# Kernel optimization log

Hardware: AMD Instinct MI355X
Metric: run time of the kernel (lower is better)

Reference implementation:

```python
import jax, jax.numpy as jnp
import numpy as np

PS = 7  # patch (window) size
NH = 8  # num heads for local attention
EPS = 1e-5


def _rel_index(ps):
    # standard Swin-style relative position index over a ps x ps window
    coords = np.stack(np.meshgrid(np.arange(ps), np.arange(ps), indexing='ij'))  # (2,ps,ps)
    flat = coords.reshape(2, -1)                                # (2, ps*ps)
    rel = (flat[:, :, None] - flat[:, None, :]).transpose(1, 2, 0)  # (N,N,2)
    rel[..., 0] += ps - 1
    rel[..., 1] += ps - 1
    rel[..., 0] *= 2 * ps - 1
    return rel.sum(-1)  # (N,N) values in [0,(2ps-1)^2)

REL_IDX = jnp.asarray(_rel_index(PS))  # (49,49)


def _mha(x, qkv_w, qkv_b, proj_w, proj_b, num_heads, bias):
    # x: (Bn, N, C); weights stored (in,out)
    Bn, N, C = x.shape
    d = C // num_heads
    qkv = (x @ qkv_w + qkv_b).reshape(Bn, N, 3, num_heads, d).transpose(2, 0, 3, 1, 4)
    q, k, v = qkv[0], qkv[1], qkv[2]
    attn = jnp.einsum('bhnd,bhmd->bhnm', q, k) * (d ** -0.5)
    if bias is not None:
        attn = attn + bias
    attn = jax.nn.softmax(attn, axis=-1)
    out = jnp.einsum('bhnm,bhmd->bhnd', attn, v).transpose(0, 2, 1, 3).reshape(Bn, N, C)
    return out @ proj_w + proj_b


def setup_inputs() -> dict:
    key = jax.random.key(0)
    ks = jax.random.split(key, 8)
    B, C, H, W = 4, 256, 112, 112
    s = 0.02
    return {
        'x': jax.random.normal(ks[0], (B, C, H, W), jnp.float32),
        'norm_gamma': jnp.ones((C,), jnp.float32),
        'norm_beta': jnp.zeros((C,), jnp.float32),
        'qkv_l_w': jax.random.normal(ks[1], (C, 3 * C), jnp.float32) * s,
        'qkv_l_b': jnp.zeros((3 * C,), jnp.float32),
        'proj_l_w': jax.random.normal(ks[2], (C, C), jnp.float32) * s,
        'proj_l_b': jnp.zeros((C,), jnp.float32),
        'rpb_table': jax.random.normal(ks[3], ((2 * PS - 1) ** 2, NH), jnp.float32) * s,
        'qkv_c_w': jax.random.normal(ks[4], (PS * PS, 3 * PS * PS), jnp.float32) * s,
        'qkv_c_b': jnp.zeros((3 * PS * PS,), jnp.float32),
        'proj_c_w': jax.random.normal(ks[5], (PS * PS, PS * PS), jnp.float32) * s,
        'proj_c_b': jnp.zeros((PS * PS,), jnp.float32),
        'proj_w': jax.random.normal(ks[6], (2 * C, C), jnp.float32) * s,
    }


def reference(x, norm_gamma, norm_beta, qkv_l_w, qkv_l_b, proj_l_w, proj_l_b,
              rpb_table, qkv_c_w, qkv_c_b, proj_c_w, proj_c_b, proj_w):
    B, C, H, W = x.shape
    ps, N = PS, PS * PS
    nP = (H // ps) * (W // ps)
    shortcut = x

    # b c h w -> b h w c, then LayerNorm over C
    xt = x.transpose(0, 2, 3, 1)
    mu = xt.mean(-1, keepdims=True)
    var = xt.var(-1, keepdims=True)
    xn = (xt - mu) * jax.lax.rsqrt(var + EPS) * norm_gamma + norm_beta

    # window partition -> (B*nP, N, C)
    patches = xn.reshape(B, H // ps, ps, W // ps, ps, C)
    patches = patches.transpose(0, 1, 3, 2, 4, 5).reshape(-1, N, C)

    # local windowed attention with relative position bias
    bias = rpb_table[REL_IDX].transpose(2, 0, 1)[None]  # (1,NH,N,N)
    attn_local = _mha(patches, qkv_l_w, qkv_l_b, proj_l_w, proj_l_b, NH, bias)

    # cross-channel attention: (B*C, nP, N), dim=N, single head, no RPE
    pc = patches.reshape(B, nP, N, C).transpose(0, 3, 1, 2).reshape(B * C, nP, N)
    attn_cross = _mha(pc, qkv_c_w, qkv_c_b, proj_c_w, proj_c_b, 1, None)
    attn_cross = attn_cross.reshape(B, C, nP, N).transpose(0, 2, 3, 1).reshape(-1, N, C)

    def reverse(w):  # (B*nP, N, C) -> (B, H*W, C)
        w = w.reshape(B, H // ps, W // ps, ps, ps, C)
        return w.transpose(0, 1, 3, 2, 4, 5).reshape(B, H * W, C)

    out = jnp.concatenate([reverse(attn_local), reverse(attn_cross)], axis=-1) @ proj_w
    out = out.reshape(B, H, W, C).transpose(0, 3, 1, 2)
    return (out, shortcut)
```

## Files before the change

### kernel.cpp

```cpp
#include <hip/hip_runtime.h>
#include <hip/hip_bf16.h>


#define PS 7
#define NWIN_N 49
#define CH 256
#define HH 112
#define WW 112
#define BB 4
#define NHEAD 8
#define HD 32

static constexpr size_t ELEMS = (size_t)BB * CH * HH * WW;
static constexpr size_t SZ    = ELEMS * 2;

typedef __attribute__((ext_vector_type(8))) short short8;
typedef __attribute__((ext_vector_type(4))) float f32x4;

static __device__ __forceinline__ unsigned short bf16_bits(float v) {
    __hip_bfloat16 h = __float2bfloat16(v);
    return *reinterpret_cast<unsigned short*>(&h);
}

static __device__ __forceinline__ void gload_lds16(const void* g, void* l) {
    __builtin_amdgcn_global_load_lds(
        (const __attribute__((address_space(1))) unsigned int*)g,
        (__attribute__((address_space(3))) unsigned int*)l, 16, 0, 0);
}

__global__ __launch_bounds__(256) void ln_partition_kernel(
    const float* __restrict__ x, const float* __restrict__ gamma,
    const float* __restrict__ beta, __hip_bfloat16* __restrict__ patches)
{
    int blk = blockIdx.x;
    int seg = blk % 7;
    int bh = blk / 7;
    int h = bh % HH, b = bh / HH;
    int w0 = seg * 16;
    int tid = threadIdx.x;

    __shared__ float X[256][17];
    __shared__ float mus[16], rstds[16];

    #pragma unroll
    for (int l = 0; l < 16; ++l) {
        int idx = l * 256 + tid;
        int c = idx >> 4, wl = idx & 15;
        X[c][wl] = x[((size_t)(b * CH + c) * HH + h) * WW + w0 + wl];
    }
    __syncthreads();

    if (tid < 16) {
        float s = 0.f, ss = 0.f;
        for (int c = 0; c < 256; ++c) { float v = X[c][tid]; s += v; ss += v * v; }
        float mu = s * (1.f / 256.f);
        float var = ss * (1.f / 256.f) - mu * mu;
        mus[tid] = mu;
        rstds[tid] = rsqrtf(var + 1e-5f);
    }
    __syncthreads();

    int c = tid;
    float g = gamma[c], be = beta[c];
    int hp = h / PS, r = h - hp * PS;
    #pragma unroll
    for (int wl = 0; wl < 16; ++wl) {
        int w = w0 + wl;
        int wp = w / PS, cc = w - wp * PS;
        int win = (b * 16 + hp) * 16 + wp;
        int i = r * PS + cc;
        float v = (X[c][wl] - mus[wl]) * rstds[wl] * g + be;
        patches[((size_t)win * NWIN_N + i) * CH + c] = __float2bfloat16(v);
    }
}

__global__ __launch_bounds__(256) void copy_f32_kernel(
    const float* __restrict__ x, float* __restrict__ out)
{
    size_t i = ((size_t)blockIdx.x * 256 + threadIdx.x) * 4;
    *(float4*)(out + i) = *(const float4*)(x + i);
}

__global__ __launch_bounds__(256) void prep_wt_kernel(
    const float* __restrict__ W, unsigned short* __restrict__ Wt,
    int Kreal, int N, int Kpad, int Npad)
{
    int idx = blockIdx.x * 256 + threadIdx.x;
    if (idx >= Npad * Kpad) return;
    int n = idx / Kpad, k = idx - n * Kpad;
    float v = (n < N && k < Kreal) ? W[(size_t)k * N + n] : 0.f;
    Wt[idx] = bf16_bits(v);
}

__global__ __launch_bounds__(256) void prep_wt_qkvc_kernel(
    const float* __restrict__ W, unsigned short* __restrict__ Wt)
{
    int idx = blockIdx.x * 256 + threadIdx.x;
    if (idx >= 192 * 64) return;
    int n = idx >> 6, k = idx & 63;
    int s = -1;
    if (n < 49) s = n;
    else if (n >= 56 && n < 105) s = n - 7;
    else if (n >= 112 && n < 161) s = n - 14;
    float v = (s >= 0 && k < 49) ? W[(size_t)k * 147 + s] : 0.f;
    Wt[idx] = bf16_bits(v);
}

__global__ __launch_bounds__(192) void prep_bias_c_kernel(
    const float* __restrict__ b, float* __restrict__ bc)
{
    int n = threadIdx.x;
    int s = -1;
    if (n < 49) s = n;
    else if (n >= 56 && n < 105) s = n - 7;
    else if (n >= 112 && n < 161) s = n - 14;
    bc[n] = (s >= 0) ? b[s] : 0.f;
}

__global__ __launch_bounds__(256) void bias_prep_kernel(
    const float* __restrict__ rpb, float* __restrict__ biasb)
{
    int idx = blockIdx.x * 256 + threadIdx.x;
    int head = idx >> 12;
    int rem = idx & 4095;
    int i = rem >> 6, j = rem & 63;
    float v;
    if (j >= NWIN_N) v = -1e9f;
    else if (i >= NWIN_N) v = 0.f;
    else {
        int ri = i / 7, ci = i - ri * 7;
        int rj = j / 7, cj = j - rj * 7;
        v = rpb[((ri - rj + 6) * 13 + (ci - cj + 6)) * NHEAD + head];
    }
    biasb[idx] = v;
}

__global__ __launch_bounds__(256) void gemm_mfma_kernel(
    const __hip_bfloat16* __restrict__ A1p, const __hip_bfloat16* __restrict__ A2p,
    int K1, const unsigned short* __restrict__ Wt, const float* __restrict__ bias,
    __hip_bfloat16* __restrict__ Cb, float* __restrict__ Cf,
    int M, int N, int K, int pitchN)
{
    __shared__ __align__(16) unsigned short Alds[128 * 64];
    __shared__ __align__(16) unsigned short Wlds[64 * 64];
    const unsigned short* A1 = (const unsigned short*)A1p;
    const unsigned short* A2 = (const unsigned short*)A2p;

    const int nb = gridDim.x;
    const int ntiles = nb * gridDim.y;
    const int bid = blockIdx.y * nb + blockIdx.x;
    const int chunk = ntiles >> 3;
    const int tile = (bid & 7) * chunk + (bid >> 3);
    const int m0 = (tile / nb) * 128, n0 = (tile % nb) * 64;

    const int tid = threadIdx.x, lane = tid & 63, wave = tid >> 6;
    const int wm = wave >> 1, wn = wave & 1;
    const int lr = lane & 15, lk = lane >> 4;

    f32x4 acc[4][2];
    #pragma unroll
    for (int i = 0; i < 4; ++i)
        #pragma unroll
        for (int j = 0; j < 2; ++j) acc[i][j] = (f32x4){0.f, 0.f, 0.f, 0.f};

    for (int k0 = 0; k0 < K; k0 += 64) {
        #pragma unroll
        for (int i = 0; i < 4; ++i) {
            int s_lin = i * 256 + tid;
            int row = s_lin >> 3, sl = s_lin & 7;
            int c8 = ((sl ^ (row & 7)) << 3);
            int k = k0 + c8;
            const unsigned short* src = (k < K1)
                ? A1 + (size_t)(m0 + row) * K1 + k
                : A2 + (size_t)(m0 + row) * (K - K1) + (k - K1);
            gload_lds16(src, Alds + (size_t)(i * 256 + wave * 64) * 8);
        }
        #pragma unroll
        for (int i = 0; i < 2; ++i) {
            int s_lin = i * 256 + tid;
            int row = s_lin >> 3, sl = s_lin & 7;
            int c8 = ((sl ^ (row & 7)) << 3);
            gload_lds16(Wt + (size_t)(n0 + row) * K + k0 + c8,
                        Wlds + (size_t)(i * 256 + wave * 64) * 8);
        }
        __syncthreads();
        #pragma unroll
        for (int kk = 0; kk < 64; kk += 32) {
            short8 a[4], w[2];
            #pragma unroll
            for (int mi = 0; mi < 4; ++mi) {
                int r = wm * 64 + mi * 16 + lr;
                int sl = (kk >> 3) + lk;
                a[mi] = *(const short8*)&Alds[(r << 6) + (((sl) ^ (r & 7)) << 3)];
            }
            #pragma unroll
            for (int nj = 0; nj < 2; ++nj) {
                int r = wn * 32 + nj * 16 + lr;
                int sl = (kk >> 3) + lk;
                w[nj] = *(const short8*)&Wlds[(r << 6) + (((sl) ^ (r & 7)) << 3)];
            }
            #pragma unroll
            for (int mi = 0; mi < 4; ++mi)
                #pragma unroll
                for (int nj = 0; nj < 2; ++nj)
                    acc[mi][nj] = __builtin_amdgcn_mfma_f32_16x16x32_bf16(
                        a[mi], w[nj], acc[mi][nj], 0, 0, 0);
        }
        __syncthreads();
    }

    if (Cb) {
        if ((pitchN & 7) == 0) {
            #pragma unroll
            for (int nj = 0; nj < 2; ++nj) {
                int n = n0 + wn * 32 + nj * 16 + lr;
                float bv = (bias && n < N) ? bias[n] : 0.f;
                int col = wn * 32 + nj * 16 + lr;
                #pragma unroll
                for (int mi = 0; mi < 4; ++mi)
                    #pragma unroll
                    for (int r = 0; r < 4; ++r) {
                        int row = wm * 64 + mi * 16 + lk * 4 + r;
                        int idx = (row << 6) + (((col >> 3) ^ (row & 7)) << 3) + (col & 7);
                        Alds[idx] = bf16_bits(acc[mi][nj][r] + bv);
                    }
            }
            __syncthreads();
            #pragma unroll
            for (int i = 0; i < 4; ++i) {
                int s = tid + 256 * i;
                int row = s >> 3, sl = s & 7;
                if (n0 + sl * 8 + 8 <= pitchN)
                    *(short8*)((unsigned short*)Cb + (size_t)(m0 + row) * pitchN + n0 + sl * 8) =
                        *(const short8*)&Alds[(row << 6) + (((sl) ^ (row & 7)) << 3)];
            }
        } else {
            #pragma unroll
            for (int nj = 0; nj < 2; ++nj) {
                int n = n0 + wn * 32 + nj * 16 + lr;
                if (n >= N) continue;
                float bv = bias ? bias[n] : 0.f;
                #pragma unroll
                for (int mi = 0; mi < 4; ++mi) {
                    #pragma unroll
                    for (int r = 0; r < 4; ++r) {
                        int m = m0 + wm * 64 + mi * 16 + lk * 4 + r;
                        ((unsigned short*)Cb)[(size_t)m * pitchN + n] =
                            bf16_bits(acc[mi][nj][r] + bv);
                    }
                }
            }
        }
    } else {
        #pragma unroll
        for (int mi = 0; mi < 4; ++mi) {
            #pragma unroll
            for (int r = 0; r < 4; ++r) {
                int m = m0 + wm * 64 + mi * 16 + lk * 4 + r;
                int b = m / 12544, rem = m - b * 12544;
                int p = rem / 49, t = rem - p * 49;
                int h = (p >> 4) * 7 + t / 7, w = (p & 15) * 7 + (t % 7);
                size_t ob = ((size_t)(b * 256) * HH + h) * WW + w;
                #pragma unroll
                for (int nj = 0; nj < 2; ++nj) {
                    int ch = n0 + wn * 32 + nj * 16 + lr;
                    Cf[ob + (size_t)ch * (HH * WW)] = acc[mi][nj][r];
                }
            }
        }
    }
}

__global__ __launch_bounds__(64) void local_attn_mfma_kernel(
    const __hip_bfloat16* __restrict__ qkv,
    const float* __restrict__ biasb,
    __hip_bfloat16* __restrict__ outp)
{
    __shared__ __align__(16) unsigned short VT_lds[32][72];
    __shared__ __align__(16) unsigned short P_lds[16][72];

    const int win  = blockIdx.x >> 3;
    const int head = blockIdx.x & 7;
    const int lane = threadIdx.x;
    const int lr = lane & 15, lk = lane >> 4;
    const unsigned short* q16 = (const unsigned short*)qkv;
    const size_t rowbase = (size_t)win * NWIN_N;
    const float scale = 0.17677669529663687f;

    for (int t = 0; t < 32; ++t) {
        int idx = lane + 64 * t;
        int j = idx >> 5, d = idx & 31;
        unsigned short v = 0;
        if (j < NWIN_N) v = q16[(rowbase + j) * 768 + 512 + head * HD + d];
        VT_lds[d][j] = v;
    }

    short8 kf[4], qf[4];
    #pragma unroll
    for (int jt = 0; jt < 4; ++jt) {
        int j = jt * 16 + lr;
        short8 f = *(const short8*)(q16 + (rowbase + j) * 768 + 256 + head * HD + lk * 8);
        if (j >= NWIN_N) {
            #pragma unroll
            for (int e = 0; e < 8; ++e) f[e] = 0;
        }
        kf[jt] = f;
    }
    #pragma unroll
    for (int it = 0; it < 4; ++it) {
        int i = it * 16 + lr;
        qf[it] = *(const short8*)(q16 + (rowbase + i) * 768 + head * HD + lk * 8);
    }
    __syncthreads();

    #pragma unroll
    for (int it = 0; it < 4; ++it) {
        const int i = it * 16 + lr;
        f32x4 sacc[4];
        #pragma unroll
        for (int jt = 0; jt < 4; ++jt) {
            f32x4 z = (f32x4){0.f, 0.f, 0.f, 0.f};
            sacc[jt] = __builtin_amdgcn_mfma_f32_16x16x32_bf16(kf[jt], qf[it], z, 0, 0, 0);
        }
        const float* brow = biasb + head * 4096 + i * 64;
        float sv[4][4];
        float mt = -1e30f;
        #pragma unroll
        for (int jt = 0; jt < 4; ++jt) {
            float4 bv = *(const float4*)&brow[jt * 16 + lk * 4];
            sv[jt][0] = sacc[jt][0] * scale + bv.x;
            sv[jt][1] = sacc[jt][1] * scale + bv.y;
            sv[jt][2] = sacc[jt][2] * scale + bv.z;
            sv[jt][3] = sacc[jt][3] * scale + bv.w;
            #pragma unroll
            for (int r = 0; r < 4; ++r) mt = fmaxf(mt, sv[jt][r]);
        }
        mt = fmaxf(mt, __shfl_xor(mt, 16, 64));
        mt = fmaxf(mt, __shfl_xor(mt, 32, 64));
        float psum = 0.f;
        #pragma unroll
        for (int jt = 0; jt < 4; ++jt) {
            float p0 = __expf(sv[jt][0] - mt);
            float p1 = __expf(sv[jt][1] - mt);
            float p2 = __expf(sv[jt][2] - mt);
            float p3 = __expf(sv[jt][3] - mt);
            psum += (p0 + p1) + (p2 + p3);
            uint2 wv;
            wv.x = (unsigned)bf16_bits(p0) | ((unsigned)bf16_bits(p1) << 16);
            wv.y = (unsigned)bf16_bits(p2) | ((unsigned)bf16_bits(p3) << 16);
            *(uint2*)&P_lds[lr][jt * 16 + lk * 4] = wv;
        }
        psum += __shfl_xor(psum, 16, 64);
        psum += __shfl_xor(psum, 32, 64);
        __syncthreads();

        f32x4 oacc[2];
        oacc[0] = (f32x4){0.f, 0.f, 0.f, 0.f};
        oacc[1] = (f32x4){0.f, 0.f, 0.f, 0.f};
        #pragma unroll
        for (int kst = 0; kst < 2; ++kst) {
            short8 bfv = *(const short8*)&P_lds[lr][kst * 32 + lk * 8];
            #pragma unroll
            for (int dt = 0; dt < 2; ++dt) {
                short8 af = *(const short8*)&VT_lds[dt * 16 + lr][kst * 32 + lk * 8];
                oacc[dt] = __builtin_amdgcn_mfma_f32_16x16x32_bf16(af, bfv, oacc[dt], 0, 0, 0);
            }
        }
        if (i < NWIN_N) {
            float inv = 1.f / psum;
            unsigned short* orow = (unsigned short*)outp + (rowbase + i) * CH + head * HD;
            #pragma unroll
            for (int dt = 0; dt < 2; ++dt) {
                uint2 wv;
                wv.x = (unsigned)bf16_bits(oacc[dt][0] * inv)
                     | ((unsigned)bf16_bits(oacc[dt][1] * inv) << 16);
                wv.y = (unsigned)bf16_bits(oacc[dt][2] * inv)
                     | ((unsigned)bf16_bits(oacc[dt][3] * inv) << 16);
                *(uint2*)&orow[dt * 16 + lk * 4] = wv;
            }
        }
        __syncthreads();
    }
}

__global__ __launch_bounds__(256) void cross_attn_mfma_kernel(
    const __hip_bfloat16* __restrict__ qkv,
    __hip_bfloat16* __restrict__ outp)
{
    __shared__ __align__(16) unsigned short K_lds[64][72];
    __shared__ __align__(16) unsigned short VT_lds[64][72];
    __shared__ __align__(16) unsigned short P_lds[2][64][72];

    const int bc = blockIdx.x;
    const size_t base = (size_t)bc * 256;
    const int tid  = threadIdx.x;
    const int lane = tid & 63;
    const int wave = tid >> 6;
    const int i0w  = wave * 64;
    const int lr   = lane & 15;
    const int lk   = lane >> 4;
    const int prow = wave * 16 + lr;

    const unsigned short* q16 = (const unsigned short*)qkv;
    const float inv7 = 1.f / 7.f;
    const short8 zf = (short8){0, 0, 0, 0, 0, 0, 0, 0};

    short8 qf[4][2];
    #pragma unroll
    for (int it = 0; it < 4; ++it) {
        const unsigned short* qrow = q16 + (base + i0w + it * 16 + lr) * 168;
        #pragma unroll
        for (int kst = 0; kst < 2; ++kst) {
            int k0 = lk * 8 + kst * 32;
            qf[it][kst] = (k0 <= 48) ? *(const short8*)(qrow + k0) : zf;
        }
    }

    float m_run[4], l_run[4];
    f32x4 acc_o[4][4];
    #pragma unroll
    for (int it = 0; it < 4; ++it) { m_run[it] = -1e30f; l_run[it] = 0.f; }
    #pragma unroll
    for (int dt = 0; dt < 4; ++dt)
        #pragma unroll
        for (int it = 0; it < 4; ++it) acc_o[dt][it] = (f32x4){0.f, 0.f, 0.f, 0.f};

    for (int jt4 = 0; jt4 < 4; ++jt4) {
        const int j0 = jt4 * 64;
        {
            const int jr = tid >> 3, c8 = (tid & 7) * 8;
            #pragma unroll
            for (int h = 0; h < 2; ++h) {
                int jj = jr + h * 32;
                const unsigned short* row = q16 + (base + j0 + jj) * 168;
                *(short8*)&K_lds[jj][c8]    = (c8 <= 48) ? *(const short8*)(row + 56 + c8) : zf;
                *(short8*)&P_lds[0][jj][c8] = (c8 <= 48) ? *(const short8*)(row + 112 + c8) : zf;
            }
        }
        __syncthreads();
        {
            const int jj = tid & 63, dg = tid >> 6;
            #pragma unroll
            for (int e = 0; e < 16; ++e) {
                int d = dg * 16 + e;
                VT_lds[d][jj] = P_lds[0][jj][d];
            }
        }
        __syncthreads();

        #pragma unroll
        for (int it = 0; it < 4; ++it) {
            unsigned short* prowp = &P_lds[it & 1][prow][0];
            f32x4 sacc[4];
            #pragma unroll
            for (int jt = 0; jt < 4; ++jt) sacc[jt] = (f32x4){0.f, 0.f, 0.f, 0.f};
            #pragma unroll
            for (int kst = 0; kst < 2; ++kst) {
                #pragma unroll
                for (int jt = 0; jt < 4; ++jt) {
                    short8 af = *(const short8*)&K_lds[jt * 16 + lr][lk * 8 + kst * 32];
                    sacc[jt] = __builtin_amdgcn_mfma_f32_16x16x32_bf16(
                        af, qf[it][kst], sacc[jt], 0, 0, 0);
                }
            }
            float mt = -1e30f;
            #pragma unroll
            for (int jt = 0; jt < 4; ++jt)
                #pragma unroll
                for (int r = 0; r < 4; ++r) mt = fmaxf(mt, sacc[jt][r]);
            mt = fmaxf(mt, __shfl_xor(mt, 16, 64));
            mt = fmaxf(mt, __shfl_xor(mt, 32, 64));
            float mnew = fmaxf(m_run[it], mt * inv7);
            float corr = __expf(m_run[it] - mnew);
            m_run[it] = mnew;
            l_run[it] *= corr;
            #pragma unroll
            for (int dt = 0; dt < 4; ++dt)
                #pragma unroll
                for (int r = 0; r < 4; ++r) acc_o[dt][it][r] *= corr;

            float psum = 0.f;
            #pragma unroll
            for (int jt = 0; jt < 4; ++jt) {
                float p0 = __expf(sacc[jt][0] * inv7 - mnew);
                float p1 = __expf(sacc[jt][1] * inv7 - mnew);
                float p2 = __expf(sacc[jt][2] * inv7 - mnew);
                float p3 = __expf(sacc[jt][3] * inv7 - mnew);
                psum += (p0 + p1) + (p2 + p3);
                uint2 wv;
                wv.x = (unsigned)bf16_bits(p0) | ((unsigned)bf16_bits(p1) << 16);
                wv.y = (unsigned)bf16_bits(p2) | ((unsigned)bf16_bits(p3) << 16);
                *(uint2*)(prowp + jt * 16 + lk * 4) = wv;
            }
            psum += __shfl_xor(psum, 16, 64);
            psum += __shfl_xor(psum, 32, 64);
            l_run[it] += psum;

            #pragma unroll
            for (int kst = 0; kst < 2; ++kst) {
                short8 bfv = *(const short8*)(prowp + kst * 32 + lk * 8);
                #pragma unroll
                for (int dt = 0; dt < 4; ++dt) {
                    short8 af = *(const short8*)&VT_lds[dt * 16 + lr][kst * 32 + lk * 8];
                    acc_o[dt][it] = __builtin_amdgcn_mfma_f32_16x16x32_bf16(
                        af, bfv, acc_o[dt][it], 0, 0, 0);
                }
            }
        }
        __syncthreads();
    }

    #pragma unroll
    for (int it = 0; it < 4; ++it) {
        float inv = 1.f / l_run[it];
        unsigned short* orow = (unsigned short*)outp + (base + i0w + it * 16 + lr) * 64;
        #pragma unroll
        for (int dt = 0; dt < 4; ++dt) {
            uint2 wv;
            wv.x = (unsigned)bf16_bits(acc_o[dt][it][0] * inv)
                 | ((unsigned)bf16_bits(acc_o[dt][it][1] * inv) << 16);
            wv.y = (unsigned)bf16_bits(acc_o[dt][it][2] * inv)
                 | ((unsigned)bf16_bits(acc_o[dt][it][3] * inv) << 16);
            *(uint2*)&orow[dt * 16 + lk * 4] = wv;
        }
    }
}

__global__ __launch_bounds__(256) void transpose_pad_kernel(
    const __hip_bfloat16* __restrict__ patches, unsigned short* __restrict__ pc_pad)
{
    __shared__ __hip_bfloat16 T[64][66];
    int b = blockIdx.z;
    int r0 = blockIdx.y * 64, c0 = blockIdx.x * 64;
    const __hip_bfloat16* s = patches + (size_t)b * 12544 * 256;
    int tid = threadIdx.x;
    int lr4 = tid >> 6, lc = tid & 63;

    #pragma unroll
    for (int l = 0; l < 16; ++l) {
        int rr = l * 4 + lr4;
        T[rr][lc] = s[(size_t)(r0 + rr) * 256 + c0 + lc];
    }
    __syncthreads();
    int r = r0 + lc;
    int p = r / 49, t = r - p * 49;
    #pragma unroll
    for (int l = 0; l < 16; ++l) {
        int cc = l * 4 + lr4;
        size_t dst = (((size_t)(b * 256 + c0 + cc) * 256) + p) * 64 + t;
        pc_pad[dst] = *(unsigned short*)&T[lc][cc];
    }
    int plo = r0 / 49, phi = (r0 + 63) / 49;
    for (int pp = plo; pp <= phi; ++pp) {
        if (pp >= 256) break;
        for (int idx = tid; idx < 64 * 15; idx += 256) {
            int cc = idx / 15, t2 = 49 + idx % 15;
            size_t dst = (((size_t)(b * 256 + c0 + cc) * 256) + pp) * 64 + t2;
            pc_pad[dst] = 0;
        }
    }
}

__global__ __launch_bounds__(256) void transpose_bf16_kernel(
    const __hip_bfloat16* __restrict__ src, __hip_bfloat16* __restrict__ dst,
    int R, int Cc)
{
    __shared__ __hip_bfloat16 T[64][66];
    int b = blockIdx.z;
    int r0 = blockIdx.y * 64, c0 = blockIdx.x * 64;
    const __hip_bfloat16* s = src + (size_t)b * R * Cc;
    __hip_bfloat16* d = dst + (size_t)b * R * Cc;
    int tid = threadIdx.x;
    int lr = tid >> 6, lc = tid & 63;

    #pragma unroll
    for (int l = 0; l < 16; ++l) {
        int rr = l * 4 + lr;
        T[rr][lc] = s[(size_t)(r0 + rr) * Cc + c0 + lc];
    }
    __syncthreads();
    #pragma unroll
    for (int l = 0; l < 16; ++l) {
        int cc = l * 4 + lr;
        d[(size_t)(c0 + cc) * R + r0 + lc] = T[lc][cc];
    }
}

__global__ void ws_marker_kernel(float* __restrict__ out0)
{
    if (threadIdx.x == 0) out0[0] = 777.0f;
}

extern "C" void kernel_launch(void* const* d_in, const int* in_sizes, int n_in,
                              void* d_out, int out_size, void* d_ws, size_t ws_size,
                              hipStream_t stream)
{
    const float* x        = (const float*)d_in[0];
    const float* gamma    = (const float*)d_in[1];
    const float* beta     = (const float*)d_in[2];
    const float* qkv_l_w  = (const float*)d_in[3];
    const float* qkv_l_b  = (const float*)d_in[4];
    const float* proj_l_w = (const float*)d_in[5];
    const float* proj_l_b = (const float*)d_in[6];
    const float* rpb      = (const float*)d_in[7];
    const float* qkv_c_w  = (const float*)d_in[8];
    const float* qkv_c_b  = (const float*)d_in[9];
    const float* proj_c_w = (const float*)d_in[10];
    const float* proj_c_b = (const float*)d_in[11];
    const float* proj_w   = (const float*)d_in[12];

    float* out0 = (float*)d_out;
    float* out1 = out0 + ELEMS;

    copy_f32_kernel<<<(int)(ELEMS / 1024), 256, 0, stream>>>(x, out1);

    char* ws = (char*)d_ws;
    if (ws_size < 6 * SZ) {
        ws_marker_kernel<<<1, 64, 0, stream>>>(out0);
        return;
    }

    const size_t P = SZ;
    __hip_bfloat16* localOut  = (__hip_bfloat16*)(ws + 0 * P);
    unsigned short* wt_qkv_l  = (unsigned short*)(ws + 0 * P);
    float*          biasb     = (float*)(ws + 0 * P + 0x80000);
    __hip_bfloat16* patches   = (__hip_bfloat16*)(ws + 1 * P);
    __hip_bfloat16* qkv_l     = (__hip_bfloat16*)(ws + 2 * P);
    __hip_bfloat16* attnL     = (__hip_bfloat16*)(ws + 5 * P);
    char*           G         = ws + 4 * P + 0xB00000;
    unsigned short* wt_proj_l = (unsigned short*)(G + 0x000000);
    unsigned short* wt_qkv_c  = (unsigned short*)(G + 0x080000);
    unsigned short* wt_proj_c = (unsigned short*)(G + 0x100000);
    unsigned short* wt_final  = (unsigned short*)(G + 0x180000);
    float*          biasc     = (float*)(G + 0x300000);
    __hip_bfloat16* pc_pad    = (__hip_bfloat16*)(ws + 6 * P - (size_t)262144 * 64 * 2);
    __hip_bfloat16* qkvc      = (__hip_bfloat16*)(ws + 1 * P);
    __hip_bfloat16* crossAttn = pc_pad;
    __hip_bfloat16* crossProj = (__hip_bfloat16*)(ws + 1 * P);
    __hip_bfloat16* crossT    = (__hip_bfloat16*)(ws + 2 * P);

    prep_wt_kernel<<<768, 256, 0, stream>>>(qkv_l_w, wt_qkv_l, 256, 768, 256, 768);
    bias_prep_kernel<<<128, 256, 0, stream>>>(rpb, biasb);
    ln_partition_kernel<<<BB * HH * 7, 256, 0, stream>>>(x, gamma, beta, patches);
    gemm_mfma_kernel<<<dim3(12, 392), 256, 0, stream>>>(
        patches, nullptr, 256, wt_qkv_l, qkv_l_b, qkv_l, nullptr, 50176, 768, 256, 768);
    local_attn_mfma_kernel<<<1024 * NHEAD, 64, 0, stream>>>(qkv_l, biasb, attnL);
    prep_wt_kernel<<<256, 256, 0, stream>>>(proj_l_w, wt_proj_l, 256, 256, 256, 256);
    prep_wt_qkvc_kernel<<<48, 256, 0, stream>>>(qkv_c_w, wt_qkv_c);
    prep_bias_c_kernel<<<1, 192, 0, stream>>>(qkv_c_b, biasc);
    prep_wt_kernel<<<16, 256, 0, stream>>>(proj_c_w, wt_proj_c, 49, 49, 64, 64);
    prep_wt_kernel<<<512, 256, 0, stream>>>(proj_w, wt_final, 512, 256, 512, 256);
    gemm_mfma_kernel<<<dim3(4, 392), 256, 0, stream>>>(
        attnL, nullptr, 256, wt_proj_l, proj_l_b, localOut, nullptr, 50176, 256, 256, 256);
    transpose_pad_kernel<<<dim3(4, 196, BB), 256, 0, stream>>>(
        patches, (unsigned short*)pc_pad);
    gemm_mfma_kernel<<<dim3(3, 2048), 256, 0, stream>>>(
        pc_pad, nullptr, 64, wt_qkv_c, biasc, qkvc, nullptr, 262144, 161, 64, 168);
    cross_attn_mfma_kernel<<<1024, 256, 0, stream>>>(qkvc, crossAttn);
    gemm_mfma_kernel<<<dim3(1, 2048), 256, 0, stream>>>(
        crossAttn, nullptr, 64, wt_proj_c, proj_c_b, crossProj, nullptr, 262144, 49, 64, 49);
    transpose_bf16_kernel<<<dim3(196, 4, BB), 256, 0, stream>>>(crossProj, crossT, 256, 12544);
    gemm_mfma_kernel<<<dim3(4, 392), 256, 0, stream>>>(
        localOut, crossT, 256, wt_final, nullptr, nullptr, out0, 50176, 256, 512, 256);
}
```

Before: 344.0 us.

## Double-buffer GEMM LDS tiles to overlap global loads with MFMA compute

Splits the A and W shared-memory tiles into two buffers and issues the next K-tile's global-to-LDS loads before computing on the current one. A partial vmcnt wait plus raw s_barrier replace the __syncthreads pair, so loads for tile t+1 can proceed while MFMAs on tile t run. This doubles LDS use (48KB), which may lower occupancy, and relies on the exact count of outstanding vector memory ops per stage (6).

```diff
diff --git a/kernel.cpp b/kernel.cpp
--- a/kernel.cpp
+++ b/kernel.cpp
@@ -141,8 +141,8 @@
     __hip_bfloat16* __restrict__ Cb, float* __restrict__ Cf,
     int M, int N, int K, int pitchN)
 {
-    __shared__ __align__(16) unsigned short Alds[128 * 64];
-    __shared__ __align__(16) unsigned short Wlds[64 * 64];
+    __shared__ __align__(16) unsigned short Alds[2][128 * 64];
+    __shared__ __align__(16) unsigned short Wlds[2][64 * 64];
     const unsigned short* A1 = (const unsigned short*)A1p;
     const unsigned short* A2 = (const unsigned short*)A2p;
 
@@ -163,7 +163,7 @@
         #pragma unroll
         for (int j = 0; j < 2; ++j) acc[i][j] = (f32x4){0.f, 0.f, 0.f, 0.f};
 
-    for (int k0 = 0; k0 < K; k0 += 64) {
+    auto stage = [&](int k0, int buf) {
         #pragma unroll
         for (int i = 0; i < 4; ++i) {
             int s_lin = i * 256 + tid;
@@ -173,7 +173,7 @@
             const unsigned short* src = (k < K1)
                 ? A1 + (size_t)(m0 + row) * K1 + k
                 : A2 + (size_t)(m0 + row) * (K - K1) + (k - K1);
-            gload_lds16(src, Alds + (size_t)(i * 256 + wave * 64) * 8);
+            gload_lds16(src, &Alds[buf][(size_t)(i * 256 + wave * 64) * 8]);
         }
         #pragma unroll
         for (int i = 0; i < 2; ++i) {
@@ -181,9 +181,22 @@
             int row = s_lin >> 3, sl = s_lin & 7;
             int c8 = ((sl ^ (row & 7)) << 3);
             gload_lds16(Wt + (size_t)(n0 + row) * K + k0 + c8,
-                        Wlds + (size_t)(i * 256 + wave * 64) * 8);
-        }
-        __syncthreads();
+                        &Wlds[buf][(size_t)(i * 256 + wave * 64) * 8]);
+        }
+    };
+
+    const int nt = K >> 6;
+    stage(0, 0);
+    for (int t = 0; t < nt; ++t) {
+        const int cur = t & 1;
+        if (t + 1 < nt) {
+            stage((t + 1) << 6, cur ^ 1);
+            asm volatile("s_waitcnt vmcnt(6)" ::: "memory");
+        } else {
+            asm volatile("s_waitcnt vmcnt(0)" ::: "memory");
+        }
+        __builtin_amdgcn_s_barrier();
+        __builtin_amdgcn_sched_barrier(0);
         #pragma unroll
         for (int kk = 0; kk < 64; kk += 32) {
             short8 a[4], w[2];
@@ -191,13 +204,13 @@
             for (int mi = 0; mi < 4; ++mi) {
                 int r = wm * 64 + mi * 16 + lr;
                 int sl = (kk >> 3) + lk;
-                a[mi] = *(const short8*)&Alds[(r << 6) + (((sl) ^ (r & 7)) << 3)];
+                a[mi] = *(const short8*)&Alds[cur][(r << 6) + (((sl) ^ (r & 7)) << 3)];
             }
             #pragma unroll
             for (int nj = 0; nj < 2; ++nj) {
                 int r = wn * 32 + nj * 16 + lr;
                 int sl = (kk >> 3) + lk;
-                w[nj] = *(const short8*)&Wlds[(r << 6) + (((sl) ^ (r & 7)) << 3)];
+                w[nj] = *(const short8*)&Wlds[cur][(r << 6) + (((sl) ^ (r & 7)) << 3)];
             }
             #pragma unroll
             for (int mi = 0; mi < 4; ++mi)
@@ -206,7 +219,8 @@
                     acc[mi][nj] = __builtin_amdgcn_mfma_f32_16x16x32_bf16(
                         a[mi], w[nj], acc[mi][nj], 0, 0, 0);
         }
-        __syncthreads();
+        __builtin_amdgcn_sched_barrier(0);
+        __builtin_amdgcn_s_barrier();
     }
 
     if (Cb) {
@@ -222,7 +236,7 @@
                     for (int r = 0; r < 4; ++r) {
                         int row = wm * 64 + mi * 16 + lk * 4 + r;
                         int idx = (row << 6) + (((col >> 3) ^ (row & 7)) << 3) + (col & 7);
-                        Alds[idx] = bf16_bits(acc[mi][nj][r] + bv);
+                        Alds[0][idx] = bf16_bits(acc[mi][nj][r] + bv);
                     }
             }
             __syncthreads();
@@ -232,7 +246,7 @@
                 int row = s >> 3, sl = s & 7;
                 if (n0 + sl * 8 + 8 <= pitchN)
                     *(short8*)((unsigned short*)Cb + (size_t)(m0 + row) * pitchN + n0 + sl * 8) =
-                        *(const short8*)&Alds[(row << 6) + (((sl) ^ (row & 7)) << 3)];
+                        *(const short8*)&Alds[0][(row << 6) + (((sl) ^ (row & 7)) << 3)];
             }
         } else {
             #pragma unroll
```

New measurement: 356.0 us. +3.5%, slower.

## Fuse cross-channel K/V projection and output projection into cross attention kernel

Applied to the files above, without the earlier changes.

The cross-channel path previously ran a separate QKV GEMM writing a padded 168-wide buffer, then attention, then a proj GEMM. Now only Q is produced by a GEMM. K and V are computed on the fly inside the attention kernel from the patch tile using MFMA, and the output projection is applied in the same kernel before writing. This removes large intermediate global writes and reads and one kernel launch. The cost is redundant K/V projection compute per block and extra LDS use, which may lower occupancy.

```diff
diff --git a/kernel.cpp b/kernel.cpp
--- a/kernel.cpp
+++ b/kernel.cpp
@@ -83,38 +83,13 @@
 
 __global__ __launch_bounds__(256) void prep_wt_kernel(
     const float* __restrict__ W, unsigned short* __restrict__ Wt,
-    int Kreal, int N, int Kpad, int Npad)
+    int Kreal, int validN, int srcPitch, int nOff, int Kpad, int Npad)
 {
     int idx = blockIdx.x * 256 + threadIdx.x;
     if (idx >= Npad * Kpad) return;
     int n = idx / Kpad, k = idx - n * Kpad;
-    float v = (n < N && k < Kreal) ? W[(size_t)k * N + n] : 0.f;
+    float v = (n < validN && k < Kreal) ? W[(size_t)k * srcPitch + nOff + n] : 0.f;
     Wt[idx] = bf16_bits(v);
-}
-
-__global__ __launch_bounds__(256) void prep_wt_qkvc_kernel(
-    const float* __restrict__ W, unsigned short* __restrict__ Wt)
-{
-    int idx = blockIdx.x * 256 + threadIdx.x;
-    if (idx >= 192 * 64) return;
-    int n = idx >> 6, k = idx & 63;
-    int s = -1;
-    if (n < 49) s = n;
-    else if (n >= 56 && n < 105) s = n - 7;
-    else if (n >= 112 && n < 161) s = n - 14;
-    float v = (s >= 0 && k < 49) ? W[(size_t)k * 147 + s] : 0.f;
-    Wt[idx] = bf16_bits(v);
-}
-
-__global__ __launch_bounds__(192) void prep_bias_c_kernel(
-    const float* __restrict__ b, float* __restrict__ bc)
-{
-    int n = threadIdx.x;
-    int s = -1;
-    if (n < 49) s = n;
-    else if (n >= 56 && n < 105) s = n - 7;
-    else if (n >= 112 && n < 161) s = n - 14;
-    bc[n] = (s >= 0) ? b[s] : 0.f;
 }
 
 __global__ __launch_bounds__(256) void bias_prep_kernel(
@@ -383,13 +358,22 @@
     }
 }
 
-__global__ __launch_bounds__(256) void cross_attn_mfma_kernel(
-    const __hip_bfloat16* __restrict__ qkv,
-    __hip_bfloat16* __restrict__ outp)
-{
-    __shared__ __align__(16) unsigned short K_lds[64][72];
-    __shared__ __align__(16) unsigned short VT_lds[64][72];
-    __shared__ __align__(16) unsigned short P_lds[2][64][72];
+__global__ __launch_bounds__(256) void cross_fused_kernel(
+    const __hip_bfloat16* __restrict__ pc,
+    const __hip_bfloat16* __restrict__ qb,
+    const unsigned short* __restrict__ wkc,
+    const unsigned short* __restrict__ wvc,
+    const unsigned short* __restrict__ wpc,
+    const float* __restrict__ qkv_c_b,
+    const float* __restrict__ proj_c_b,
+    __hip_bfloat16* __restrict__ crossProj)
+{
+    __shared__ __align__(16) unsigned short SMEM[5 * 64 * 72];
+    unsigned short* A_lds  = SMEM;
+    unsigned short* K_lds  = SMEM + 1 * 64 * 72;
+    unsigned short* VT_lds = SMEM + 2 * 64 * 72;
+    unsigned short* P0     = SMEM + 3 * 64 * 72;
+    unsigned short* P1     = SMEM + 4 * 64 * 72;
 
     const int bc = blockIdx.x;
     const size_t base = (size_t)bc * 256;
@@ -401,19 +385,17 @@
     const int lk   = lane >> 4;
     const int prow = wave * 16 + lr;
 
-    const unsigned short* q16 = (const unsigned short*)qkv;
+    const unsigned short* pc16 = (const unsigned short*)pc;
+    const unsigned short* q16  = (const unsigned short*)qb;
     const float inv7 = 1.f / 7.f;
-    const short8 zf = (short8){0, 0, 0, 0, 0, 0, 0, 0};
 
     short8 qf[4][2];
     #pragma unroll
     for (int it = 0; it < 4; ++it) {
-        const unsigned short* qrow = q16 + (base + i0w + it * 16 + lr) * 168;
-        #pragma unroll
-        for (int kst = 0; kst < 2; ++kst) {
-            int k0 = lk * 8 + kst * 32;
-            qf[it][kst] = (k0 <= 48) ? *(const short8*)(qrow + k0) : zf;
-        }
+        const unsigned short* qrow = q16 + (base + i0w + it * 16 + lr) * 64;
+        #pragma unroll
+        for (int kst = 0; kst < 2; ++kst)
+            qf[it][kst] = *(const short8*)(qrow + lk * 8 + kst * 32);
     }
 
     float m_run[4], l_run[4];
@@ -432,25 +414,51 @@
             #pragma unroll
             for (int h = 0; h < 2; ++h) {
                 int jj = jr + h * 32;
-                const unsigned short* row = q16 + (base + j0 + jj) * 168;
-                *(short8*)&K_lds[jj][c8]    = (c8 <= 48) ? *(const short8*)(row + 56 + c8) : zf;
-                *(short8*)&P_lds[0][jj][c8] = (c8 <= 48) ? *(const short8*)(row + 112 + c8) : zf;
+                *(short8*)&A_lds[jj * 72 + c8] =
+                    *(const short8*)(pc16 + (base + j0 + jj) * 64 + c8);
             }
         }
         __syncthreads();
         {
-            const int jj = tid & 63, dg = tid >> 6;
-            #pragma unroll
-            for (int e = 0; e < 16; ++e) {
-                int d = dg * 16 + e;
-                VT_lds[d][jj] = P_lds[0][jj][d];
+            const int jt = wave;
+            #pragma unroll
+            for (int kt = 0; kt < 4; ++kt) {
+                f32x4 z = (f32x4){0.f, 0.f, 0.f, 0.f};
+                #pragma unroll
+                for (int kst = 0; kst < 2; ++kst) {
+                    short8 af = *(const short8*)&A_lds[(jt * 16 + lr) * 72 + lk * 8 + kst * 32];
+                    short8 wf = *(const short8*)(wkc + (kt * 16 + lr) * 64 + lk * 8 + kst * 32);
+                    z = __builtin_amdgcn_mfma_f32_16x16x32_bf16(af, wf, z, 0, 0, 0);
+                }
+                int kd = kt * 16 + lr;
+                float bv = (kd < 49) ? qkv_c_b[49 + kd] : 0.f;
+                #pragma unroll
+                for (int r = 0; r < 4; ++r)
+                    K_lds[(jt * 16 + lk * 4 + r) * 72 + kd] = bf16_bits(z[r] + bv);
+            }
+            const int vt = wave;
+            #pragma unroll
+            for (int jt2 = 0; jt2 < 4; ++jt2) {
+                f32x4 z = (f32x4){0.f, 0.f, 0.f, 0.f};
+                #pragma unroll
+                for (int kst = 0; kst < 2; ++kst) {
+                    short8 wf = *(const short8*)(wvc + (vt * 16 + lr) * 64 + lk * 8 + kst * 32);
+                    short8 af = *(const short8*)&A_lds[(jt2 * 16 + lr) * 72 + lk * 8 + kst * 32];
+                    z = __builtin_amdgcn_mfma_f32_16x16x32_bf16(wf, af, z, 0, 0, 0);
+                }
+                #pragma unroll
+                for (int r = 0; r < 4; ++r) {
+                    int vd = vt * 16 + lk * 4 + r;
+                    float bv = (vd < 49) ? qkv_c_b[98 + vd] : 0.f;
+                    VT_lds[vd * 72 + jt2 * 16 + lr] = bf16_bits(z[r] + bv);
+                }
             }
         }
         __syncthreads();
 
         #pragma unroll
         for (int it = 0; it < 4; ++it) {
-            unsigned short* prowp = &P_lds[it & 1][prow][0];
+            unsigned short* prowp = ((it & 1) ? P1 : P0) + prow * 72;
             f32x4 sacc[4];
             #pragma unroll
             for (int jt = 0; jt < 4; ++jt) sacc[jt] = (f32x4){0.f, 0.f, 0.f, 0.f};
@@ -458,7 +466,7 @@
             for (int kst = 0; kst < 2; ++kst) {
                 #pragma unroll
                 for (int jt = 0; jt < 4; ++jt) {
-                    short8 af = *(const short8*)&K_lds[jt * 16 + lr][lk * 8 + kst * 32];
+                    short8 af = *(const short8*)&K_lds[(jt * 16 + lr) * 72 + lk * 8 + kst * 32];
                     sacc[jt] = __builtin_amdgcn_mfma_f32_16x16x32_bf16(
                         af, qf[it][kst], sacc[jt], 0, 0, 0);
                 }
@@ -501,7 +509,7 @@
                 short8 bfv = *(const short8*)(prowp + kst * 32 + lk * 8);
                 #pragma unroll
                 for (int dt = 0; dt < 4; ++dt) {
-                    short8 af = *(const short8*)&VT_lds[dt * 16 + lr][kst * 32 + lk * 8];
+                    short8 af = *(const short8*)&VT_lds[(dt * 16 + lr) * 72 + kst * 32 + lk * 8];
                     acc_o[dt][it] = __builtin_amdgcn_mfma_f32_16x16x32_bf16(
                         af, bfv, acc_o[dt][it], 0, 0, 0);
                 }
@@ -510,19 +518,45 @@
         __syncthreads();
     }
 
+    unsigned short* Orow = SMEM + (1 + wave) * 64 * 72;
     #pragma unroll
     for (int it = 0; it < 4; ++it) {
         float inv = 1.f / l_run[it];
-        unsigned short* orow = (unsigned short*)outp + (base + i0w + it * 16 + lr) * 64;
-        #pragma unroll
-        for (int dt = 0; dt < 4; ++dt) {
-            uint2 wv;
-            wv.x = (unsigned)bf16_bits(acc_o[dt][it][0] * inv)
-                 | ((unsigned)bf16_bits(acc_o[dt][it][1] * inv) << 16);
-            wv.y = (unsigned)bf16_bits(acc_o[dt][it][2] * inv)
-                 | ((unsigned)bf16_bits(acc_o[dt][it][3] * inv) << 16);
-            *(uint2*)&orow[dt * 16 + lk * 4] = wv;
-        }
+        #pragma unroll
+        for (int dt = 0; dt < 4; ++dt)
+            #pragma unroll
+            for (int r = 0; r < 4; ++r)
+                Orow[(it * 16 + lr) * 72 + dt * 16 + lk * 4 + r] =
+                    bf16_bits(acc_o[dt][it][r] * inv);
+    }
+    __syncthreads();
+
+    unsigned short* orow_out = (unsigned short*)crossProj + (size_t)bc * 12544;
+    #pragma unroll
+    for (int pt = 0; pt < 4; ++pt) {
+        short8 bfr[2];
+        #pragma unroll
+        for (int kst = 0; kst < 2; ++kst)
+            bfr[kst] = *(const short8*)&Orow[(pt * 16 + lr) * 72 + lk * 8 + kst * 32];
+        f32x4 accy[4];
+        #pragma unroll
+        for (int tt = 0; tt < 4; ++tt) accy[tt] = (f32x4){0.f, 0.f, 0.f, 0.f};
+        #pragma unroll
+        for (int kst = 0; kst < 2; ++kst)
+            #pragma unroll
+            for (int tt = 0; tt < 4; ++tt) {
+                short8 wf = *(const short8*)(wpc + (tt * 16 + lr) * 64 + lk * 8 + kst * 32);
+                accy[tt] = __builtin_amdgcn_mfma_f32_16x16x32_bf16(wf, bfr[kst], accy[tt], 0, 0, 0);
+            }
+        int p = i0w + pt * 16 + lr;
+        #pragma unroll
+        for (int tt = 0; tt < 4; ++tt)
+            #pragma unroll
+            for (int r = 0; r < 4; ++r) {
+                int t = tt * 16 + lk * 4 + r;
+                if (t < 49)
+                    orow_out[p * 49 + t] = bf16_bits(accy[tt][r] + proj_c_b[t]);
+            }
     }
 }
 
@@ -629,36 +663,36 @@
     __hip_bfloat16* attnL     = (__hip_bfloat16*)(ws + 5 * P);
     char*           G         = ws + 4 * P + 0xB00000;
     unsigned short* wt_proj_l = (unsigned short*)(G + 0x000000);
-    unsigned short* wt_qkv_c  = (unsigned short*)(G + 0x080000);
-    unsigned short* wt_proj_c = (unsigned short*)(G + 0x100000);
-    unsigned short* wt_final  = (unsigned short*)(G + 0x180000);
-    float*          biasc     = (float*)(G + 0x300000);
+    unsigned short* wt_qc     = (unsigned short*)(G + 0x080000);
+    unsigned short* wt_kc     = (unsigned short*)(G + 0x090000);
+    unsigned short* wt_vc     = (unsigned short*)(G + 0x0A0000);
+    unsigned short* wt_pc     = (unsigned short*)(G + 0x0B0000);
+    unsigned short* wt_final  = (unsigned short*)(G + 0x100000);
     __hip_bfloat16* pc_pad    = (__hip_bfloat16*)(ws + 6 * P - (size_t)262144 * 64 * 2);
-    __hip_bfloat16* qkvc      = (__hip_bfloat16*)(ws + 1 * P);
-    __hip_bfloat16* crossAttn = pc_pad;
-    __hip_bfloat16* crossProj = (__hip_bfloat16*)(ws + 1 * P);
+    __hip_bfloat16* qkvc_q    = (__hip_bfloat16*)(ws + 1 * P);
+    __hip_bfloat16* crossProj = (__hip_bfloat16*)(ws + 3 * P);
     __hip_bfloat16* crossT    = (__hip_bfloat16*)(ws + 2 * P);
 
-    prep_wt_kernel<<<768, 256, 0, stream>>>(qkv_l_w, wt_qkv_l, 256, 768, 256, 768);
+    prep_wt_kernel<<<768, 256, 0, stream>>>(qkv_l_w, wt_qkv_l, 256, 768, 768, 0, 256, 768);
     bias_prep_kernel<<<128, 256, 0, stream>>>(rpb, biasb);
     ln_partition_kernel<<<BB * HH * 7, 256, 0, stream>>>(x, gamma, beta, patches);
     gemm_mfma_kernel<<<dim3(12, 392), 256, 0, stream>>>(
         patches, nullptr, 256, wt_qkv_l, qkv_l_b, qkv_l, nullptr, 50176, 768, 256, 768);
     local_attn_mfma_kernel<<<1024 * NHEAD, 64, 0, stream>>>(qkv_l, biasb, attnL);
-    prep_wt_kernel<<<256, 256, 0, stream>>>(proj_l_w, wt_proj_l, 256, 256, 256, 256);
-    prep_wt_qkvc_kernel<<<48, 256, 0, stream>>>(qkv_c_w, wt_qkv_c);
-    prep_bias_c_kernel<<<1, 192, 0, stream>>>(qkv_c_b, biasc);
-    prep_wt_kernel<<<16, 256, 0, stream>>>(proj_c_w, wt_proj_c, 49, 49, 64, 64);
-    prep_wt_kernel<<<512, 256, 0, stream>>>(proj_w, wt_final, 512, 256, 512, 256);
+    prep_wt_kernel<<<256, 256, 0, stream>>>(proj_l_w, wt_proj_l, 256, 256, 256, 0, 256, 256);
+    prep_wt_kernel<<<16, 256, 0, stream>>>(qkv_c_w, wt_qc, 49, 49, 147, 0, 64, 64);
+    prep_wt_kernel<<<16, 256, 0, stream>>>(qkv_c_w, wt_kc, 49, 49, 147, 49, 64, 64);
+    prep_wt_kernel<<<16, 256, 0, stream>>>(qkv_c_w, wt_vc, 49, 49, 147, 98, 64, 64);
+    prep_wt_kernel<<<16, 256, 0, stream>>>(proj_c_w, wt_pc, 49, 49, 49, 0, 64, 64);
+    prep_wt_kernel<<<512, 256, 0, stream>>>(proj_w, wt_final, 512, 256, 256, 0, 512, 256);
     gemm_mfma_kernel<<<dim3(4, 392), 256, 0, stream>>>(
         attnL, nullptr, 256, wt_proj_l, proj_l_b, localOut, nullptr, 50176, 256, 256, 256);
     transpose_pad_kernel<<<dim3(4, 196, BB), 256, 0, stream>>>(
         patches, (unsigned short*)pc_pad);
-    gemm_mfma_kernel<<<dim3(3, 2048), 256, 0, stream>>>(
-        pc_pad, nullptr, 64, wt_qkv_c, biasc, qkvc, nullptr, 262144, 161, 64, 168);
-    cross_attn_mfma_kernel<<<1024, 256, 0, stream>>>(qkvc, crossAttn);
     gemm_mfma_kernel<<<dim3(1, 2048), 256, 0, stream>>>(
-        crossAttn, nullptr, 64, wt_proj_c, proj_c_b, crossProj, nullptr, 262144, 49, 64, 49);
+        pc_pad, nullptr, 64, wt_qc, qkv_c_b, qkvc_q, nullptr, 262144, 49, 64, 64);
+    cross_fused_kernel<<<1024, 256, 0, stream>>>(
+        pc_pad, qkvc_q, wt_kc, wt_vc, wt_pc, qkv_c_b, proj_c_b, crossProj);
     transpose_bf16_kernel<<<dim3(196, 4, BB), 256, 0, stream>>>(crossProj, crossT, 256, 12544);
     gemm_mfma_kernel<<<dim3(4, 392), 256, 0, stream>>>(
         localOut, crossT, 256, wt_final, nullptr, nullptr, out0, 50176, 256, 512, 256);
```

New measurement: 361.6 us. 5.1% more time.
